# Kernel optimization log

Hardware: AMD Instinct MI355X
Metric: run time of the kernel (lower is better)

The kernel has to match this reference:

```python
import jax, jax.numpy as jnp
import numpy as np


def setup_inputs() -> dict:
    key = jax.random.key(0)
    k1, k2 = jax.random.split(key)
    B, C, T = 64, 16, 32768
    y_pred = jax.random.normal(k1, (B, C, T), dtype=jnp.float32)
    y_true = jax.random.normal(k2, (B, C, T), dtype=jnp.float32)
    return {"y_pred": y_pred, "y_true": y_true}


def reference(y_pred, y_true):
    # Original: for i in 1..T, sum |cumsum(pred[:,:,:i]) - cumsum(true[:,:,:i])|, mean over batch.
    # Prefix position t (0-indexed) appears in all outer iterations i >= t+1, i.e. (T - t) times.
    # => total = mean_b sum_{c,t} |cumsum(pred - true)[b,c,t]| * (T - t)
    B, C, T = y_pred.shape
    c = jnp.cumsum(y_pred - y_true, axis=2)          # (B, C, T)
    w = (T - jnp.arange(T)).astype(y_pred.dtype)     # weight T-t for position t
    total = jnp.sum(jnp.abs(c) * w, axis=(1, 2))     # (B,)
    total = jnp.mean(total)
    scaling = 2.0 / (T * C * (T * C + 1))            # apply_scaling_factor=True
    return scaling * total
```

## Files before the change

### kernel.cpp

```cpp
#include <hip/hip_runtime.h>

#define B_BATCH 64
#define C_CH    16
#define T_LEN   32768
#define THREADS 256
#define VEC     4
#define CHUNK   (THREADS * VEC)
#define NCHUNK  (T_LEN / CHUNK)
#define NROWS   (B_BATCH * C_CH)

__global__ __launch_bounds__(THREADS) void wloss_scan_kernel(
    const float* __restrict__ pred,
    const float* __restrict__ tru,
    double* __restrict__ ws_accum)
{
    const int row  = blockIdx.x;
    const int tid  = threadIdx.x;
    const int lane = tid & 63;
    const int wave = tid >> 6;

    const float4* p4 = (const float4*)(pred + (size_t)row * T_LEN);
    const float4* t4 = (const float4*)(tru  + (size_t)row * T_LEN);

    __shared__ float wtot[2][4];

    float  carry = 0.0f;
    double acc   = 0.0;

    for (int ch = 0; ch < NCHUNK; ++ch) {
        const int v4idx = ch * (CHUNK / VEC) + tid;
        float4 p = p4[v4idx];
        float4 t = t4[v4idx];

        float d0 = p.x - t.x;
        float d1 = p.y - t.y;
        float d2 = p.z - t.z;
        float d3 = p.w - t.w;

        float s1 = d0;
        float s2 = s1 + d1;
        float s3 = s2 + d2;
        float s4 = s3 + d3;

        float v = s4;
        #pragma unroll
        for (int off = 1; off < 64; off <<= 1) {
            float u = __shfl_up(v, off, 64);
            if (lane >= off) v += u;
        }

        const int par = ch & 1;
        if (lane == 63) wtot[par][wave] = v;
        __syncthreads();

        float wprefix = 0.0f;
        float total   = 0.0f;
        #pragma unroll
        for (int w = 0; w < 4; ++w) {
            float wt = wtot[par][w];
            if (w < wave) wprefix += wt;
            total += wt;
        }

        const float excl = carry + wprefix + (v - s4);

        const int   e  = ch * CHUNK + tid * VEC;
        const float w0 = (float)(T_LEN - e);

        float c1 = excl + s1;
        float c2 = excl + s2;
        float c3 = excl + s3;
        float c4 = excl + s4;

        float part = fabsf(c1) * w0
                   + fabsf(c2) * (w0 - 1.0f)
                   + fabsf(c3) * (w0 - 2.0f)
                   + fabsf(c4) * (w0 - 3.0f);
        acc += (double)part;

        carry += total;
    }

    #pragma unroll
    for (int off = 32; off > 0; off >>= 1)
        acc += __shfl_down(acc, off, 64);

    __shared__ double dtot[4];
    if (lane == 0) dtot[wave] = acc;
    __syncthreads();

    if (tid == 0) {
        double s = dtot[0] + dtot[1] + dtot[2] + dtot[3];
        atomicAdd(ws_accum, s);
    }
}

__global__ void wloss_finalize_kernel(const double* __restrict__ ws_accum,
                                      float* __restrict__ out)
{
    const double tc      = (double)T_LEN * (double)C_CH;
    const double scaling = 2.0 / (tc * (tc + 1.0));
    out[0] = (float)(ws_accum[0] * scaling / (double)B_BATCH);
}

extern "C" void kernel_launch(void* const* d_in, const int* in_sizes, int n_in,
                              void* d_out, int out_size, void* d_ws, size_t ws_size,
                              hipStream_t stream)
{
    const float* pred = (const float*)d_in[0];
    const float* tru  = (const float*)d_in[1];
    double*      ws   = (double*)d_ws;
    float*       out  = (float*)d_out;

    hipMemsetAsync(ws, 0, sizeof(double), stream);

    wloss_scan_kernel<<<NROWS, THREADS, 0, stream>>>(pred, tru, ws);
    wloss_finalize_kernel<<<1, 1, 0, stream>>>(ws, out);
}
```

Measured before the change: 280.3 us.

## Split rows into tiles with decoupled look-back scan and fuse finalize

Each row is split into 8 tiles of 4096 elements, one block per tile, so the grid grows from 1024 to 8192 blocks. The cross-tile prefix carry is resolved with a decoupled look-back over flagged slots in workspace, and block IDs come from an atomic ticket to avoid deadlock. Each thread now holds 16 elements in registers instead of looping over chunks with a barrier per chunk. The separate finalize kernel is replaced by a last-block-done counter. The cost is spin-waiting on global atomics and a larger memset.

```diff
diff --git a/kernel.cpp b/kernel.cpp
--- a/kernel.cpp
+++ b/kernel.cpp
@@ -4,103 +4,130 @@
 #define C_CH    16
 #define T_LEN   32768
 #define THREADS 256
-#define VEC     4
-#define CHUNK   (THREADS * VEC)
-#define NCHUNK  (T_LEN / CHUNK)
+#define TPT     16
+#define TILE    (THREADS * TPT)
+#define GSEG    (T_LEN / TILE)
 #define NROWS   (B_BATCH * C_CH)
+#define NBLOCKS (NROWS * GSEG)
 
-__global__ __launch_bounds__(THREADS) void wloss_scan_kernel(
+#define WS_BYTES (16 + NBLOCKS * 8)
+
+__device__ __forceinline__ unsigned long long pack_slot(unsigned int flag, float v) {
+    return ((unsigned long long)flag << 32) | (unsigned long long)__float_as_uint(v);
+}
+
+__global__ __launch_bounds__(THREADS) void wloss_lookback_kernel(
     const float* __restrict__ pred,
     const float* __restrict__ tru,
-    double* __restrict__ ws_accum)
+    void* __restrict__ ws,
+    float* __restrict__ out)
 {
-    const int row  = blockIdx.x;
+    double*             accum   = (double*)ws;
+    unsigned int*       ticket  = (unsigned int*)((char*)ws + 8);
+    unsigned int*       donecnt = (unsigned int*)((char*)ws + 12);
+    unsigned long long* slots   = (unsigned long long*)((char*)ws + 16);
+
+    __shared__ unsigned int s_bid;
+    __shared__ float  s_wtot[4];
+    __shared__ float  s_carry;
+    __shared__ double s_dtot[4];
+
     const int tid  = threadIdx.x;
     const int lane = tid & 63;
     const int wave = tid >> 6;
 
-    const float4* p4 = (const float4*)(pred + (size_t)row * T_LEN);
-    const float4* t4 = (const float4*)(tru  + (size_t)row * T_LEN);
+    if (tid == 0) s_bid = atomicAdd(ticket, 1u);
+    __syncthreads();
+    const unsigned int bid = s_bid;
+    const int row = (int)(bid >> 3);
+    const int g   = (int)(bid & (GSEG - 1));
 
-    __shared__ float wtot[2][4];
+    const float4* p4 = (const float4*)(pred + (size_t)row * T_LEN + (size_t)g * TILE) + tid * 4;
+    const float4* t4 = (const float4*)(tru  + (size_t)row * T_LEN + (size_t)g * TILE) + tid * 4;
 
-    float  carry = 0.0f;
-    double acc   = 0.0;
+    float d[TPT];
+    #pragma unroll
+    for (int k = 0; k < 4; ++k) {
+        float4 p = p4[k];
+        float4 t = t4[k];
+        d[4*k+0] = p.x - t.x;
+        d[4*k+1] = p.y - t.y;
+        d[4*k+2] = p.z - t.z;
+        d[4*k+3] = p.w - t.w;
+    }
+    #pragma unroll
+    for (int j = 1; j < TPT; ++j) d[j] += d[j-1];
 
-    for (int ch = 0; ch < NCHUNK; ++ch) {
-        const int v4idx = ch * (CHUNK / VEC) + tid;
-        float4 p = p4[v4idx];
-        float4 t = t4[v4idx];
+    float v = d[TPT-1];
+    #pragma unroll
+    for (int off = 1; off < 64; off <<= 1) {
+        float u = __shfl_up(v, off, 64);
+        if (lane >= off) v += u;
+    }
+    if (lane == 63) s_wtot[wave] = v;
+    __syncthreads();
 
-        float d0 = p.x - t.x;
-        float d1 = p.y - t.y;
-        float d2 = p.z - t.z;
-        float d3 = p.w - t.w;
+    float wprefix = 0.f, btot = 0.f;
+    #pragma unroll
+    for (int w = 0; w < 4; ++w) {
+        float wt = s_wtot[w];
+        if (w < wave) wprefix += wt;
+        btot += wt;
+    }
+    const float texcl = wprefix + (v - d[TPT-1]);
 
-        float s1 = d0;
-        float s2 = s1 + d1;
-        float s3 = s2 + d2;
-        float s4 = s3 + d3;
+    if (tid == 0) {
+        float carry = 0.f;
+        if (g == 0) {
+            atomicExch(&slots[bid], pack_slot(2u, btot));
+        } else {
+            if (g != GSEG - 1)
+                atomicExch(&slots[bid], pack_slot(1u, btot));
+            const unsigned int rbase = bid - (unsigned int)g;
+            int j = g - 1;
+            for (;;) {
+                unsigned long long s = atomicAdd(&slots[rbase + j], 0ULL);
+                unsigned int flag = (unsigned int)(s >> 32);
+                if (flag == 0u) { __builtin_amdgcn_s_sleep(1); continue; }
+                carry += __uint_as_float((unsigned int)s);
+                if (flag == 2u || j == 0) break;
+                --j;
+            }
+            if (g != GSEG - 1)
+                atomicExch(&slots[bid], pack_slot(2u, carry + btot));
+        }
+        s_carry = carry;
+    }
+    __syncthreads();
 
-        float v = s4;
-        #pragma unroll
-        for (int off = 1; off < 64; off <<= 1) {
-            float u = __shfl_up(v, off, 64);
-            if (lane >= off) v += u;
-        }
+    const float excl = s_carry + texcl;
+    const int   e0   = g * TILE + tid * TPT;
+    const float w0   = (float)(T_LEN - e0);
+    float part = 0.f;
+    #pragma unroll
+    for (int j = 0; j < TPT; ++j)
+        part += fabsf(excl + d[j]) * (w0 - (float)j);
 
-        const int par = ch & 1;
-        if (lane == 63) wtot[par][wave] = v;
-        __syncthreads();
-
-        float wprefix = 0.0f;
-        float total   = 0.0f;
-        #pragma unroll
-        for (int w = 0; w < 4; ++w) {
-            float wt = wtot[par][w];
-            if (w < wave) wprefix += wt;
-            total += wt;
-        }
-
-        const float excl = carry + wprefix + (v - s4);
-
-        const int   e  = ch * CHUNK + tid * VEC;
-        const float w0 = (float)(T_LEN - e);
-
-        float c1 = excl + s1;
-        float c2 = excl + s2;
-        float c3 = excl + s3;
-        float c4 = excl + s4;
-
-        float part = fabsf(c1) * w0
-                   + fabsf(c2) * (w0 - 1.0f)
-                   + fabsf(c3) * (w0 - 2.0f)
-                   + fabsf(c4) * (w0 - 3.0f);
-        acc += (double)part;
-
-        carry += total;
-    }
-
+    double acc = (double)part;
     #pragma unroll
     for (int off = 32; off > 0; off >>= 1)
         acc += __shfl_down(acc, off, 64);
-
-    __shared__ double dtot[4];
-    if (lane == 0) dtot[wave] = acc;
+    if (lane == 0) s_dtot[wave] = acc;
     __syncthreads();
 
     if (tid == 0) {
-        double s = dtot[0] + dtot[1] + dtot[2] + dtot[3];
-        atomicAdd(ws_accum, s);
+        double sum = s_dtot[0] + s_dtot[1] + s_dtot[2] + s_dtot[3];
+        atomicAdd(accum, sum);
+        __threadfence();
+        unsigned int done = atomicAdd(donecnt, 1u);
+        if (done == NBLOCKS - 1) {
+            __threadfence();
+            double tot = atomicAdd(accum, 0.0);
+            const double tc      = (double)T_LEN * (double)C_CH;
+            const double scaling = 2.0 / (tc * (tc + 1.0));
+            out[0] = (float)(tot * scaling / (double)B_BATCH);
+        }
     }
-}
-
-__global__ void wloss_finalize_kernel(const double* __restrict__ ws_accum,
-                                      float* __restrict__ out)
-{
-    const double tc      = (double)T_LEN * (double)C_CH;
-    const double scaling = 2.0 / (tc * (tc + 1.0));
-    out[0] = (float)(ws_accum[0] * scaling / (double)B_BATCH);
 }
 
 extern "C" void kernel_launch(void* const* d_in, const int* in_sizes, int n_in,
@@ -109,11 +136,8 @@
 {
     const float* pred = (const float*)d_in[0];
     const float* tru  = (const float*)d_in[1];
-    double*      ws   = (double*)d_ws;
-    float*       out  = (float*)d_out;
 
-    hipMemsetAsync(ws, 0, sizeof(double), stream);
+    hipMemsetAsync(d_ws, 0, WS_BYTES, stream);
 
-    wloss_scan_kernel<<<NROWS, THREADS, 0, stream>>>(pred, tru, ws);
-    wloss_finalize_kernel<<<1, 1, 0, stream>>>(ws, out);
+    wloss_lookback_kernel<<<NBLOCKS, THREADS, 0, stream>>>(pred, tru, d_ws, (float*)d_out);
 }
```

New measurement: 642.1 us. 129% more time.

## Batch eight chunks per phase to cut block barriers in row scan

Applied to the files above, without the earlier changes.

Groups eight chunks per phase. Wave-local prefix sums go to shared memory, and a single wave then scans all chunk/wave totals before the weighted abs pass. This cuts block-wide barriers from one per chunk to two per eight chunks and issues more independent loads per thread. It also replaces the atomic accumulation and memset with per-row partials reduced by a 256-thread finalize kernel. The cost is 32KB of shared memory per block, which may limit occupancy, plus extra LDS traffic.

```diff
diff --git a/kernel.cpp b/kernel.cpp
--- a/kernel.cpp
+++ b/kernel.cpp
@@ -7,13 +7,21 @@
 #define VEC     4
 #define CHUNK   (THREADS * VEC)
 #define NCHUNK  (T_LEN / CHUNK)
+#define CPP     8
+#define NPH     (NCHUNK / CPP)
+#define PHEL    (CPP * CHUNK)
 #define NROWS   (B_BATCH * C_CH)
 
-__global__ __launch_bounds__(THREADS) void wloss_scan_kernel(
+__global__ __launch_bounds__(THREADS, 4) void wloss_scan_kernel(
     const float* __restrict__ pred,
     const float* __restrict__ tru,
-    double* __restrict__ ws_accum)
+    double* __restrict__ partials)
 {
+    __shared__ float  s_pref[PHEL];
+    __shared__ float  s_wt[CPP * 4];
+    __shared__ float  s_rowc;
+    __shared__ double s_d[4];
+
     const int row  = blockIdx.x;
     const int tid  = threadIdx.x;
     const int lane = tid & 63;
@@ -22,64 +30,81 @@
     const float4* p4 = (const float4*)(pred + (size_t)row * T_LEN);
     const float4* t4 = (const float4*)(tru  + (size_t)row * T_LEN);
 
-    __shared__ float wtot[2][4];
+    if (tid == 0) s_rowc = 0.0f;
+    double acc = 0.0;
 
-    float  carry = 0.0f;
-    double acc   = 0.0;
+    for (int ph = 0; ph < NPH; ++ph) {
+        if (ph) __syncthreads();
 
-    for (int ch = 0; ch < NCHUNK; ++ch) {
-        const int v4idx = ch * (CHUNK / VEC) + tid;
-        float4 p = p4[v4idx];
-        float4 t = t4[v4idx];
+        #pragma unroll
+        for (int c8 = 0; c8 < CPP; ++c8) {
+            const int c   = ph * CPP + c8;
+            const int idx = c * (CHUNK / VEC) + tid;
+            float4 p = p4[idx];
+            float4 t = t4[idx];
+            float d0 = p.x - t.x, d1 = p.y - t.y, d2 = p.z - t.z, d3 = p.w - t.w;
+            float s1 = d0, s2 = s1 + d1, s3 = s2 + d2, s4 = s3 + d3;
 
-        float d0 = p.x - t.x;
-        float d1 = p.y - t.y;
-        float d2 = p.z - t.z;
-        float d3 = p.w - t.w;
-
-        float s1 = d0;
-        float s2 = s1 + d1;
-        float s3 = s2 + d2;
-        float s4 = s3 + d3;
-
-        float v = s4;
-        #pragma unroll
-        for (int off = 1; off < 64; off <<= 1) {
-            float u = __shfl_up(v, off, 64);
-            if (lane >= off) v += u;
+            float v = s4;
+            #pragma unroll
+            for (int off = 1; off < 64; off <<= 1) {
+                float u = __shfl_up(v, off, 64);
+                if (lane >= off) v += u;
+            }
+            const float we = v - s4;
+            float4 st = { we + s1, we + s2, we + s3, we + s4 };
+            *(float4*)&s_pref[c8 * CHUNK + tid * VEC] = st;
+            if (lane == 63) s_wt[c8 * 4 + wave] = v;
         }
-
-        const int par = ch & 1;
-        if (lane == 63) wtot[par][wave] = v;
         __syncthreads();
 
-        float wprefix = 0.0f;
-        float total   = 0.0f;
+        if (wave == 0) {
+            float val = (lane < 32) ? s_wt[lane] : 0.0f;
+            float inc = val;
+            #pragma unroll
+            for (int off = 1; off < 32; off <<= 1) {
+                float u = __shfl_up(inc, off, 64);
+                if (lane >= off) inc += u;
+            }
+            const float rc = s_rowc;
+            if (lane < 32) s_wt[lane] = rc + inc - val;
+            if (lane == 31) s_rowc = rc + inc;
+        }
+        __syncthreads();
+
         #pragma unroll
-        for (int w = 0; w < 4; ++w) {
-            float wt = wtot[par][w];
-            if (w < wave) wprefix += wt;
-            total += wt;
+        for (int c8 = 0; c8 < CPP; ++c8) {
+            const float carry = s_wt[c8 * 4 + wave];
+            float4 pr = *(const float4*)&s_pref[c8 * CHUNK + tid * VEC];
+            const int   e0 = (ph * CPP + c8) * CHUNK + tid * VEC;
+            const float w0 = (float)(T_LEN - e0);
+            float part = fabsf(carry + pr.x) * w0
+                       + fabsf(carry + pr.y) * (w0 - 1.0f)
+                       + fabsf(carry + pr.z) * (w0 - 2.0f)
+                       + fabsf(carry + pr.w) * (w0 - 3.0f);
+            acc += (double)part;
         }
+    }
 
-        const float excl = carry + wprefix + (v - s4);
+    #pragma unroll
+    for (int off = 32; off > 0; off >>= 1)
+        acc += __shfl_down(acc, off, 64);
+    if (lane == 0) s_d[wave] = acc;
+    __syncthreads();
 
-        const int   e  = ch * CHUNK + tid * VEC;
-        const float w0 = (float)(T_LEN - e);
+    if (tid == 0)
+        partials[row] = s_d[0] + s_d[1] + s_d[2] + s_d[3];
+}
 
-        float c1 = excl + s1;
-        float c2 = excl + s2;
-        float c3 = excl + s3;
-        float c4 = excl + s4;
+__global__ __launch_bounds__(THREADS) void wloss_finalize_kernel(
+    const double* __restrict__ partials, float* __restrict__ out)
+{
+    const int tid  = threadIdx.x;
+    const int lane = tid & 63;
+    const int wave = tid >> 6;
 
-        float part = fabsf(c1) * w0
-                   + fabsf(c2) * (w0 - 1.0f)
-                   + fabsf(c3) * (w0 - 2.0f)
-                   + fabsf(c4) * (w0 - 3.0f);
-        acc += (double)part;
-
-        carry += total;
-    }
+    double acc = 0.0;
+    for (int i = tid; i < NROWS; i += THREADS) acc += partials[i];
 
     #pragma unroll
     for (int off = 32; off > 0; off >>= 1)
@@ -90,17 +115,11 @@
     __syncthreads();
 
     if (tid == 0) {
-        double s = dtot[0] + dtot[1] + dtot[2] + dtot[3];
-        atomicAdd(ws_accum, s);
+        const double tot     = dtot[0] + dtot[1] + dtot[2] + dtot[3];
+        const double tc      = (double)T_LEN * (double)C_CH;
+        const double scaling = 2.0 / (tc * (tc + 1.0));
+        out[0] = (float)(tot * scaling / (double)B_BATCH);
     }
-}
-
-__global__ void wloss_finalize_kernel(const double* __restrict__ ws_accum,
-                                      float* __restrict__ out)
-{
-    const double tc      = (double)T_LEN * (double)C_CH;
-    const double scaling = 2.0 / (tc * (tc + 1.0));
-    out[0] = (float)(ws_accum[0] * scaling / (double)B_BATCH);
 }
 
 extern "C" void kernel_launch(void* const* d_in, const int* in_sizes, int n_in,
@@ -109,11 +128,9 @@
 {
     const float* pred = (const float*)d_in[0];
     const float* tru  = (const float*)d_in[1];
-    double*      ws   = (double*)d_ws;
-    float*       out  = (float*)d_out;
+    double*      partials = (double*)d_ws;
+    float*       out      = (float*)d_out;
 
-    hipMemsetAsync(ws, 0, sizeof(double), stream);
-
-    wloss_scan_kernel<<<NROWS, THREADS, 0, stream>>>(pred, tru, ws);
-    wloss_finalize_kernel<<<1, 1, 0, stream>>>(ws, out);
+    wloss_scan_kernel<<<NROWS, THREADS, 0, stream>>>(pred, tru, partials);
+    wloss_finalize_kernel<<<1, THREADS, 0, stream>>>(partials, out);
 }
```

Measured after the change: 279.8 us. No clear change (-0.2%).

## Use single-wave per-row scan with software-pipelined loads and no block syncs

Applied to the files above, without the earlier changes.

Each row is now scanned by one 64-lane wave instead of a 256-thread block, which removes the shared-memory wave-total exchange and the per-chunk __syncthreads. Each lane now handles 8 elements per step. Loads for up to eight 512-element steps are kept in flight through double-buffered register groups, aiming to hide memory latency. The atomicAdd and memset are replaced by per-row partials that a 256-thread finalize kernel reduces. In exchange, only 1024 waves run in total, so occupancy is low and the kernel relies on register-held loads to keep memory busy.

```diff
diff --git a/kernel.cpp b/kernel.cpp
--- a/kernel.cpp
+++ b/kernel.cpp
@@ -3,83 +3,112 @@
 #define B_BATCH 64
 #define C_CH    16
 #define T_LEN   32768
-#define THREADS 256
-#define VEC     4
-#define CHUNK   (THREADS * VEC)
-#define NCHUNK  (T_LEN / CHUNK)
 #define NROWS   (B_BATCH * C_CH)
+#define STEP    512
+#define NSTEP   (T_LEN / STEP)
 
-__global__ __launch_bounds__(THREADS) void wloss_scan_kernel(
+
+struct Quad { float4 p0, p1, t0, t1; };
+
+__device__ __forceinline__ Quad ldstep(const float4* __restrict__ P,
+                                       const float4* __restrict__ Tq, int s) {
+    Quad q;
+    q.p0 = P [s * 128];
+    q.p1 = P [s * 128 + 1];
+    q.t0 = Tq[s * 128];
+    q.t1 = Tq[s * 128 + 1];
+    return q;
+}
+
+__global__ __launch_bounds__(64, 1) void wloss_row_kernel(
     const float* __restrict__ pred,
     const float* __restrict__ tru,
-    double* __restrict__ ws_accum)
+    double* __restrict__ partials)
 {
     const int row  = blockIdx.x;
+    const int lane = threadIdx.x;
+
+    const float4* P  = (const float4*)(pred + (size_t)row * T_LEN) + lane * 2;
+    const float4* Tq = (const float4*)(tru  + (size_t)row * T_LEN) + lane * 2;
+
+    float  carry = 0.0f;
+    double acc   = 0.0;
+
+#define PROC(q, sidx)                                                        \
+    {                                                                        \
+        float d0 = (q).p0.x - (q).t0.x;                                      \
+        float d1 = (q).p0.y - (q).t0.y;                                      \
+        float d2 = (q).p0.z - (q).t0.z;                                      \
+        float d3 = (q).p0.w - (q).t0.w;                                      \
+        float d4 = (q).p1.x - (q).t1.x;                                      \
+        float d5 = (q).p1.y - (q).t1.y;                                      \
+        float d6 = (q).p1.z - (q).t1.z;                                      \
+        float d7 = (q).p1.w - (q).t1.w;                                      \
+        d1 += d0; d2 += d1; d3 += d2; d4 += d3; d5 += d4; d6 += d5; d7 += d6;\
+        float v = d7;                                                        \
+        _Pragma("unroll")                                                    \
+        for (int off = 1; off < 64; off <<= 1) {                             \
+            float u = __shfl_up(v, off, 64);                                 \
+            if (lane >= off) v += u;                                         \
+        }                                                                    \
+        const float total = __shfl(v, 63, 64);                               \
+        const float excl  = carry + (v - d7);                                \
+        const float w0    = (float)(T_LEN - ((sidx) * STEP + lane * 8));     \
+        float part = fabsf(excl + d0) *  w0                                  \
+                   + fabsf(excl + d1) * (w0 - 1.0f)                          \
+                   + fabsf(excl + d2) * (w0 - 2.0f)                          \
+                   + fabsf(excl + d3) * (w0 - 3.0f)                          \
+                   + fabsf(excl + d4) * (w0 - 4.0f)                          \
+                   + fabsf(excl + d5) * (w0 - 5.0f)                          \
+                   + fabsf(excl + d6) * (w0 - 6.0f)                          \
+                   + fabsf(excl + d7) * (w0 - 7.0f);                         \
+        acc   += (double)part;                                               \
+        carry += total;                                                      \
+    }
+
+    Quad a0 = ldstep(P, Tq, 0);
+    Quad a1 = ldstep(P, Tq, 1);
+    Quad a2 = ldstep(P, Tq, 2);
+    Quad a3 = ldstep(P, Tq, 3);
+
+    for (int g = 0; g < NSTEP - 8; g += 8) {
+        Quad b0 = ldstep(P, Tq, g + 4);
+        Quad b1 = ldstep(P, Tq, g + 5);
+        Quad b2 = ldstep(P, Tq, g + 6);
+        Quad b3 = ldstep(P, Tq, g + 7);
+        PROC(a0, g + 0); PROC(a1, g + 1); PROC(a2, g + 2); PROC(a3, g + 3);
+        a0 = ldstep(P, Tq, g + 8);
+        a1 = ldstep(P, Tq, g + 9);
+        a2 = ldstep(P, Tq, g + 10);
+        a3 = ldstep(P, Tq, g + 11);
+        PROC(b0, g + 4); PROC(b1, g + 5); PROC(b2, g + 6); PROC(b3, g + 7);
+    }
+    {
+        const int g = NSTEP - 8;
+        Quad b0 = ldstep(P, Tq, g + 4);
+        Quad b1 = ldstep(P, Tq, g + 5);
+        Quad b2 = ldstep(P, Tq, g + 6);
+        Quad b3 = ldstep(P, Tq, g + 7);
+        PROC(a0, g + 0); PROC(a1, g + 1); PROC(a2, g + 2); PROC(a3, g + 3);
+        PROC(b0, g + 4); PROC(b1, g + 5); PROC(b2, g + 6); PROC(b3, g + 7);
+    }
+#undef PROC
+
+    #pragma unroll
+    for (int off = 32; off > 0; off >>= 1)
+        acc += __shfl_down(acc, off, 64);
+    if (lane == 0) partials[row] = acc;
+}
+
+__global__ __launch_bounds__(256) void wloss_finalize_kernel(
+    const double* __restrict__ partials, float* __restrict__ out)
+{
     const int tid  = threadIdx.x;
     const int lane = tid & 63;
     const int wave = tid >> 6;
 
-    const float4* p4 = (const float4*)(pred + (size_t)row * T_LEN);
-    const float4* t4 = (const float4*)(tru  + (size_t)row * T_LEN);
-
-    __shared__ float wtot[2][4];
-
-    float  carry = 0.0f;
-    double acc   = 0.0;
-
-    for (int ch = 0; ch < NCHUNK; ++ch) {
-        const int v4idx = ch * (CHUNK / VEC) + tid;
-        float4 p = p4[v4idx];
-        float4 t = t4[v4idx];
-
-        float d0 = p.x - t.x;
-        float d1 = p.y - t.y;
-        float d2 = p.z - t.z;
-        float d3 = p.w - t.w;
-
-        float s1 = d0;
-        float s2 = s1 + d1;
-        float s3 = s2 + d2;
-        float s4 = s3 + d3;
-
-        float v = s4;
-        #pragma unroll
-        for (int off = 1; off < 64; off <<= 1) {
-            float u = __shfl_up(v, off, 64);
-            if (lane >= off) v += u;
-        }
-
-        const int par = ch & 1;
-        if (lane == 63) wtot[par][wave] = v;
-        __syncthreads();
-
-        float wprefix = 0.0f;
-        float total   = 0.0f;
-        #pragma unroll
-        for (int w = 0; w < 4; ++w) {
-            float wt = wtot[par][w];
-            if (w < wave) wprefix += wt;
-            total += wt;
-        }
-
-        const float excl = carry + wprefix + (v - s4);
-
-        const int   e  = ch * CHUNK + tid * VEC;
-        const float w0 = (float)(T_LEN - e);
-
-        float c1 = excl + s1;
-        float c2 = excl + s2;
-        float c3 = excl + s3;
-        float c4 = excl + s4;
-
-        float part = fabsf(c1) * w0
-                   + fabsf(c2) * (w0 - 1.0f)
-                   + fabsf(c3) * (w0 - 2.0f)
-                   + fabsf(c4) * (w0 - 3.0f);
-        acc += (double)part;
-
-        carry += total;
-    }
+    double acc = 0.0;
+    for (int i = tid; i < NROWS; i += 256) acc += partials[i];
 
     #pragma unroll
     for (int off = 32; off > 0; off >>= 1)
@@ -90,17 +119,11 @@
     __syncthreads();
 
     if (tid == 0) {
-        double s = dtot[0] + dtot[1] + dtot[2] + dtot[3];
-        atomicAdd(ws_accum, s);
+        const double tot     = dtot[0] + dtot[1] + dtot[2] + dtot[3];
+        const double tc      = (double)T_LEN * (double)C_CH;
+        const double scaling = 2.0 / (tc * (tc + 1.0));
+        out[0] = (float)(tot * scaling / (double)B_BATCH);
     }
-}
-
-__global__ void wloss_finalize_kernel(const double* __restrict__ ws_accum,
-                                      float* __restrict__ out)
-{
-    const double tc      = (double)T_LEN * (double)C_CH;
-    const double scaling = 2.0 / (tc * (tc + 1.0));
-    out[0] = (float)(ws_accum[0] * scaling / (double)B_BATCH);
 }
 
 extern "C" void kernel_launch(void* const* d_in, const int* in_sizes, int n_in,
@@ -109,11 +132,9 @@
 {
     const float* pred = (const float*)d_in[0];
     const float* tru  = (const float*)d_in[1];
-    double*      ws   = (double*)d_ws;
-    float*       out  = (float*)d_out;
+    double* partials  = (double*)d_ws;
+    float*  out       = (float*)d_out;
 
-    hipMemsetAsync(ws, 0, sizeof(double), stream);
-
-    wloss_scan_kernel<<<NROWS, THREADS, 0, stream>>>(pred, tru, ws);
-    wloss_finalize_kernel<<<1, 1, 0, stream>>>(ws, out);
+    wloss_row_kernel     <<<NROWS, 64, 0, stream>>>(pred, tru, partials);
+    wloss_finalize_kernel<<<1,    256, 0, stream>>>(partials, out);
 }
```

Result: no change. 283.4 us (+1.1%).
